# Kernel tuning notes

Measured on AMD Instinct MI355X. Metric: run time of the kernel, lower is better.

## Reference

```python
import jax, jax.numpy as jnp
import numpy as np
import math

D_MODEL = 1024
NUM_HEADS = 16
HEAD_DIM = D_MODEL // NUM_HEADS


def setup_inputs() -> dict:
    key = jax.random.key(0)
    k1, k2, k3, k4 = jax.random.split(key, 4)
    x = jax.random.normal(k1, (1, 4096, D_MODEL), dtype=jnp.float32)
    # torch nn.Linear weights: [out_features, in_features]
    s = 1.0 / math.sqrt(D_MODEL)
    w_qkv = jax.random.uniform(k2, (3 * D_MODEL, D_MODEL), jnp.float32, -s, s)
    w_out = jax.random.uniform(k3, (D_MODEL, D_MODEL), jnp.float32, -s, s)
    b_out = jax.random.uniform(k4, (D_MODEL,), jnp.float32, -s, s)
    return {"x": x, "w_qkv": w_qkv, "w_out": w_out, "b_out": b_out}


def reference(x, w_qkv, w_out, b_out):
    B, T, C = x.shape
    qkv = (x @ w_qkv.T).reshape(B, T, 3, NUM_HEADS, HEAD_DIM)
    q, k, v = qkv[:, :, 0], qkv[:, :, 1], qkv[:, :, 2]  # [B,T,H,Dh]
    scores = jnp.einsum('bthd,bshd->bhts', q, k) / jnp.sqrt(jnp.float32(HEAD_DIM))
    weights = jax.nn.softmax(scores, axis=-1)  # [B,H,T,S]
    attn = jnp.einsum('bhts,bshd->bthd', weights, v).reshape(B, T, C)
    return attn @ w_out.T + b_out
```

## Files before the change

kernel.cpp:

```cpp
#include <hip/hip_runtime.h>
#include <hip/hip_bf16.h>
#include <math.h>

#define T_SEQ 4096
#define NH 16
#define HD 64
#define C_DIM 1024
#define N_QKV 3072

typedef __bf16 bf16x8 __attribute__((ext_vector_type(8)));
typedef __bf16 bf16x2 __attribute__((ext_vector_type(2)));
typedef float f32x4 __attribute__((ext_vector_type(4)));
typedef float f32x16 __attribute__((ext_vector_type(16)));
typedef unsigned short u16x8 __attribute__((ext_vector_type(8)));
typedef unsigned short u16x4 __attribute__((ext_vector_type(4)));
typedef unsigned int u32x4 __attribute__((ext_vector_type(4)));

__device__ __forceinline__ unsigned short f2bf(float f) {
  unsigned u = __builtin_bit_cast(unsigned, f);
  u += 0x7FFFu + ((u >> 16) & 1u);
  return (unsigned short)(u >> 16);
}

__device__ __forceinline__ bf16x8 lds_frag(const unsigned short* p) {
  return __builtin_bit_cast(bf16x8, *reinterpret_cast<const u16x8*>(p));
}

__global__ void convert_kernel(const float* __restrict__ x,
                               const float* __restrict__ wqkv,
                               const float* __restrict__ wout,
                               unsigned short* __restrict__ xb,
                               unsigned short* __restrict__ wqkvb,
                               unsigned short* __restrict__ woutb) {
  const int NX = T_SEQ * C_DIM;
  const int NW = N_QKV * C_DIM;
  const int NO = C_DIM * C_DIM;
  int idx = blockIdx.x * blockDim.x + threadIdx.x;
  int i = idx * 4;
  if (i >= NX + NW + NO) return;
  const float* src;
  unsigned short* dst;
  if (i < NX)            { src = x + i;                dst = xb + i; }
  else if (i < NX + NW)  { src = wqkv + (i - NX);      dst = wqkvb + (i - NX); }
  else                   { src = wout + (i - NX - NW); dst = woutb + (i - NX - NW); }
  float4 v = *reinterpret_cast<const float4*>(src);
  u16x4 o;
  o[0] = f2bf(v.x); o[1] = f2bf(v.y); o[2] = f2bf(v.z); o[3] = f2bf(v.w);
  *reinterpret_cast<u16x4*>(dst) = o;
}

template <bool F32OUT>
__global__ __launch_bounds__(256) void gemm_bt(
    const unsigned short* __restrict__ A, const unsigned short* __restrict__ Bm,
    unsigned short* __restrict__ Cb, float* __restrict__ Cf,
    const float* __restrict__ bias, int M, int N, int K,
    int scale_cols, float ascale) {
  __shared__ __align__(16) unsigned short As[128 * 64];
  __shared__ __align__(16) unsigned short Bs[128 * 64];
  const int tid = threadIdx.x;
  const int lane = tid & 63, wid = tid >> 6;
  const int l15 = lane & 15, g = lane >> 4;
  const int nbn = N >> 7;
  const int bm = blockIdx.x / nbn, bn = blockIdx.x % nbn;
  const int wm = wid >> 1, wn = wid & 1;

  f32x4 acc[4][4];
  const f32x4 zero = {0.f, 0.f, 0.f, 0.f};
#pragma unroll
  for (int m = 0; m < 4; m++)
#pragma unroll
    for (int n = 0; n < 4; n++) acc[m][n] = zero;

  for (int k0 = 0; k0 < K; k0 += 64) {
    __syncthreads();
#pragma unroll
    for (int i = 0; i < 4; i++) {
      int c = tid + i * 256;
      int row = c >> 3, slot = c & 7;
      int b_off = row * 128 + ((slot * 16) ^ ((row & 7) << 4));
      u16x8 va = *reinterpret_cast<const u16x8*>(A + (size_t)(bm * 128 + row) * K + k0 + slot * 8);
      *reinterpret_cast<u16x8*>(reinterpret_cast<char*>(As) + b_off) = va;
      u16x8 vb = *reinterpret_cast<const u16x8*>(Bm + (size_t)(bn * 128 + row) * K + k0 + slot * 8);
      *reinterpret_cast<u16x8*>(reinterpret_cast<char*>(Bs) + b_off) = vb;
    }
    __syncthreads();
#pragma unroll
    for (int kk = 0; kk < 2; kk++) {
      bf16x8 af[4], bfr[4];
#pragma unroll
      for (int m = 0; m < 4; m++) {
        int row = wm * 64 + m * 16 + l15;
        af[m] = lds_frag(reinterpret_cast<const unsigned short*>(
            reinterpret_cast<const char*>(As) + row * 128 + ((kk * 64 + g * 16) ^ ((l15 & 7) << 4))));
      }
#pragma unroll
      for (int n = 0; n < 4; n++) {
        int row = wn * 64 + n * 16 + l15;
        bfr[n] = lds_frag(reinterpret_cast<const unsigned short*>(
            reinterpret_cast<const char*>(Bs) + row * 128 + ((kk * 64 + g * 16) ^ ((l15 & 7) << 4))));
      }
#pragma unroll
      for (int m = 0; m < 4; m++)
#pragma unroll
        for (int n = 0; n < 4; n++)
          acc[m][n] = __builtin_amdgcn_mfma_f32_16x16x32_bf16(af[m], bfr[n], acc[m][n], 0, 0, 0);
    }
  }
#pragma unroll
  for (int m = 0; m < 4; m++) {
    int row0 = bm * 128 + wm * 64 + m * 16 + g * 4;
#pragma unroll
    for (int n = 0; n < 4; n++) {
      int col = bn * 128 + wn * 64 + n * 16 + l15;
      float bi = 0.f;
      if (F32OUT) bi = bias[col];
      float cs = (col < scale_cols) ? ascale : 1.0f;
#pragma unroll
      for (int r = 0; r < 4; r++) {
        float v = acc[m][n][r];
        if (F32OUT) Cf[(size_t)(row0 + r) * N + col] = v + bi;
        else        Cb[(size_t)(row0 + r) * N + col] = f2bf(v * cs);
      }
    }
  }
}

__global__ __launch_bounds__(512, 4) void attn_kernel(
    const unsigned short* __restrict__ qkv,
    unsigned short* __restrict__ attn) {
  __shared__ __align__(16) unsigned short Ksh[2][2][64 * 72];
  __shared__ __align__(16) unsigned short Vsh[2][2][64 * 72];
  const int tid = threadIdx.x;
  const int lane = tid & 63, wid = tid >> 6;
  const int qw = wid & 3, str = wid >> 2;
  const int stid = qw * 64 + lane;
  const int l31 = lane & 31, hi = lane >> 5;
  const int sw = (blockIdx.x & 7) * 64 + (blockIdx.x >> 3);
  const int h = sw >> 5;
  const int qb = sw & 31;
  const int t0 = qb * 128 + qw * 32;
  const int q = l31;
  const int kvbase = str * (T_SEQ / 2);
  const int NT = T_SEQ / 128;

  const int krow = stid >> 3, kslot = stid & 7;
  const int kp = stid & 31, d0 = (stid >> 5) * 8;

  bf16x8 qf[4];
#pragma unroll
  for (int ds = 0; ds < 4; ds++) {
    const unsigned short* p = qkv + (size_t)(t0 + q) * N_QKV + h * HD + ds * 16 + hi * 8;
    qf[ds] = __builtin_bit_cast(bf16x8, *reinterpret_cast<const u16x8*>(p));
  }

  float l_run = 0.f;
  f32x16 o[2];
  const f32x16 zero16 = {0.f};
  o[0] = zero16; o[1] = zero16;
  f32x16 minit;
#pragma unroll
  for (int i = 0; i < 16; i++) minit[i] = -4.0f;

  u16x8 kreg[2], vreg[2];
  {
    const int kv0 = kvbase;
#pragma unroll
    for (int i = 0; i < 2; i++)
      kreg[i] = *reinterpret_cast<const u16x8*>(
          qkv + (size_t)(kv0 + krow + i * 32) * N_QKV + C_DIM + h * HD + kslot * 8);
    const unsigned short* vsrc =
        qkv + (size_t)(kv0 + 2 * kp) * N_QKV + 2 * C_DIM + h * HD + d0;
    vreg[0] = *reinterpret_cast<const u16x8*>(vsrc);
    vreg[1] = *reinterpret_cast<const u16x8*>(vsrc + N_QKV);
  }

  for (int t = 0; t < NT; t++) {
    unsigned short* Kb = Ksh[str][t & 1];
    unsigned short* Vb = Vsh[str][t & 1];
#pragma unroll
    for (int i = 0; i < 2; i++)
      *reinterpret_cast<u16x8*>(&Kb[(krow + i * 32) * 72 + kslot * 8]) = kreg[i];
#pragma unroll
    for (int j = 0; j < 8; j++) {
      unsigned pk = (unsigned)vreg[0][j] | ((unsigned)vreg[1][j] << 16);
      *reinterpret_cast<unsigned*>(&Vb[(d0 + j) * 72 + 2 * kp]) = pk;
    }
    if (t < NT - 1) {
      const int kv0 = kvbase + (t + 1) * 64;
#pragma unroll
      for (int i = 0; i < 2; i++)
        kreg[i] = *reinterpret_cast<const u16x8*>(
            qkv + (size_t)(kv0 + krow + i * 32) * N_QKV + C_DIM + h * HD + kslot * 8);
      const unsigned short* vsrc =
          qkv + (size_t)(kv0 + 2 * kp) * N_QKV + 2 * C_DIM + h * HD + d0;
      vreg[0] = *reinterpret_cast<const u16x8*>(vsrc);
      vreg[1] = *reinterpret_cast<const u16x8*>(vsrc + N_QKV);
    }
    __syncthreads();

    f32x16 s[2];
#pragma unroll
    for (int nt = 0; nt < 2; nt++) {
      s[nt] = minit;
#pragma unroll
      for (int ds = 0; ds < 4; ds++) {
        bf16x8 kf = lds_frag(&Kb[(nt * 32 + l31) * 72 + ds * 16 + hi * 8]);
        s[nt] = __builtin_amdgcn_mfma_f32_32x32x16_bf16(kf, qf[ds], s[nt], 0, 0, 0);
      }
    }

    unsigned wA[2][8];
    float psum[16];
#pragma unroll
    for (int nt = 0; nt < 2; nt++)
#pragma unroll
      for (int i = 0; i < 8; i++) {
        float pa = __builtin_amdgcn_exp2f(s[nt][2 * i]);
        float pb = __builtin_amdgcn_exp2f(s[nt][2 * i + 1]);
        bf16x2 pk = {(__bf16)pa, (__bf16)pb};
        wA[nt][i] = __builtin_bit_cast(unsigned, pk);
        psum[nt * 8 + i] = pa + pb;
      }
#pragma unroll
    for (int i = 0; i < 8; i++) psum[i] += psum[i + 8];
#pragma unroll
    for (int i = 0; i < 4; i++) psum[i] += psum[i + 4];
    l_run += (psum[0] + psum[2]) + (psum[1] + psum[3]);

#pragma unroll
    for (int nt = 0; nt < 2; nt++)
#pragma unroll
      for (int base = 0; base < 8; base += 4)
#pragma unroll
        for (int k = 0; k < 2; k++) {
          unsigned A = wA[nt][base + k];
          unsigned B = wA[nt][base + k + 2];
          unsigned snd = hi ? A : B;
          unsigned rcv = __shfl_xor(snd, 32);
          wA[nt][base + k]     = hi ? rcv : A;
          wA[nt][base + k + 2] = hi ? B   : rcv;
        }

#pragma unroll
    for (int nt = 0; nt < 2; nt++) {
      u32x4 f0 = {wA[nt][0], wA[nt][1], wA[nt][2], wA[nt][3]};
      u32x4 f1 = {wA[nt][4], wA[nt][5], wA[nt][6], wA[nt][7]};
      bf16x8 pf0 = __builtin_bit_cast(bf16x8, f0);
      bf16x8 pf1 = __builtin_bit_cast(bf16x8, f1);
#pragma unroll
      for (int dblk = 0; dblk < 2; dblk++) {
        bf16x8 vf0 = lds_frag(&Vb[(dblk * 32 + l31) * 72 + nt * 32 + hi * 8]);
        o[dblk] = __builtin_amdgcn_mfma_f32_32x32x16_bf16(vf0, pf0, o[dblk], 0, 0, 0);
        bf16x8 vf1 = lds_frag(&Vb[(dblk * 32 + l31) * 72 + nt * 32 + 16 + hi * 8]);
        o[dblk] = __builtin_amdgcn_mfma_f32_32x32x16_bf16(vf1, pf1, o[dblk], 0, 0, 0);
      }
    }
  }

  __syncthreads();
  float* ob = reinterpret_cast<float*>(&Ksh[0][0][0]);
  float* lb = reinterpret_cast<float*>(&Vsh[0][0][0]);
  const int midx = qw * 64 + lane;
  if (str == 1) {
#pragma unroll
    for (int dblk = 0; dblk < 2; dblk++)
#pragma unroll
      for (int r = 0; r < 16; r++)
        ob[(dblk * 16 + r) * 256 + midx] = o[dblk][r];
    lb[midx] = l_run;
  }
  __syncthreads();
  if (str == 0) {
#pragma unroll
    for (int dblk = 0; dblk < 2; dblk++)
#pragma unroll
      for (int r = 0; r < 16; r++)
        o[dblk][r] += ob[(dblk * 16 + r) * 256 + midx];
    l_run += lb[midx];

    float inv = 1.f / (l_run + __shfl_xor(l_run, 32));
    const int t = t0 + q;
#pragma unroll
    for (int dblk = 0; dblk < 2; dblk++)
#pragma unroll
      for (int qd = 0; qd < 4; qd++) {
        u16x4 w;
#pragma unroll
        for (int i = 0; i < 4; i++) w[i] = f2bf(o[dblk][qd * 4 + i] * inv);
        *reinterpret_cast<u16x4*>(
            &attn[(size_t)t * C_DIM + h * HD + dblk * 32 + qd * 8 + hi * 4]) = w;
      }
  }
}

extern "C" void kernel_launch(void* const* d_in, const int* in_sizes, int n_in,
                              void* d_out, int out_size, void* d_ws, size_t ws_size,
                              hipStream_t stream) {
  const float* x     = (const float*)d_in[0];
  const float* w_qkv = (const float*)d_in[1];
  const float* w_out = (const float*)d_in[2];
  const float* b_out = (const float*)d_in[3];
  float* out = (float*)d_out;
  char* ws = (char*)d_ws;
  unsigned short* xb    = (unsigned short*)(ws);
  unsigned short* wqkvb = (unsigned short*)(ws + (8u << 20));
  unsigned short* woutb = (unsigned short*)(ws + (14u << 20));
  unsigned short* qkvb  = (unsigned short*)(ws + (16u << 20));
  unsigned short* attnb = (unsigned short*)(ws + (40u << 20));

  const float QSCALE = 0.125f * 1.44269504f;

  convert_kernel<<<8192, 256, 0, stream>>>(x, w_qkv, w_out, xb, wqkvb, woutb);
  gemm_bt<false><<<768, 256, 0, stream>>>(xb, wqkvb, qkvb, nullptr, nullptr,
                                          T_SEQ, N_QKV, C_DIM, C_DIM, QSCALE);
  attn_kernel<<<512, 512, 0, stream>>>(qkvb, attnb);
  gemm_bt<true><<<256, 256, 0, stream>>>(attnb, woutb, nullptr, out, b_out,
                                         T_SEQ, C_DIM, C_DIM, 0, 1.0f);
}
```

Baseline: 173.9 us.

## Process two query tiles per wave in attention to reuse K/V fragments

```diff
diff --git a/kernel.cpp b/kernel.cpp
--- a/kernel.cpp
+++ b/kernel.cpp
@@ -125,171 +125,201 @@
   }
 }
 
-__global__ __launch_bounds__(512, 4) void attn_kernel(
+__global__ __launch_bounds__(256, 2) void attn_kernel(
     const unsigned short* __restrict__ qkv,
     unsigned short* __restrict__ attn) {
   __shared__ __align__(16) unsigned short Ksh[2][2][64 * 72];
   __shared__ __align__(16) unsigned short Vsh[2][2][64 * 72];
   const int tid = threadIdx.x;
   const int lane = tid & 63, wid = tid >> 6;
-  const int qw = wid & 3, str = wid >> 2;
+  const int qw = wid & 1, str = wid >> 1;
   const int stid = qw * 64 + lane;
   const int l31 = lane & 31, hi = lane >> 5;
   const int sw = (blockIdx.x & 7) * 64 + (blockIdx.x >> 3);
   const int h = sw >> 5;
   const int qb = sw & 31;
-  const int t0 = qb * 128 + qw * 32;
+  const int t0 = qb * 128 + qw * 64;
   const int q = l31;
   const int kvbase = str * (T_SEQ / 2);
   const int NT = T_SEQ / 128;
 
-  const int krow = stid >> 3, kslot = stid & 7;
-  const int kp = stid & 31, d0 = (stid >> 5) * 8;
-
-  bf16x8 qf[4];
-#pragma unroll
-  for (int ds = 0; ds < 4; ds++) {
-    const unsigned short* p = qkv + (size_t)(t0 + q) * N_QKV + h * HD + ds * 16 + hi * 8;
-    qf[ds] = __builtin_bit_cast(bf16x8, *reinterpret_cast<const u16x8*>(p));
-  }
-
-  float l_run = 0.f;
-  f32x16 o[2];
+  const int krow = stid >> 1, ks4 = (stid & 1) * 4;
+  const int kp = stid & 31, d0 = (stid >> 5) * 16;
+
+  bf16x8 qf[2][4];
+#pragma unroll
+  for (int j = 0; j < 2; j++)
+#pragma unroll
+    for (int ds = 0; ds < 4; ds++) {
+      const unsigned short* p =
+          qkv + (size_t)(t0 + j * 32 + q) * N_QKV + h * HD + ds * 16 + hi * 8;
+      qf[j][ds] = __builtin_bit_cast(bf16x8, *reinterpret_cast<const u16x8*>(p));
+    }
+
+  float l_run[2] = {0.f, 0.f};
+  f32x16 o[2][2];
   const f32x16 zero16 = {0.f};
-  o[0] = zero16; o[1] = zero16;
+  o[0][0] = zero16; o[0][1] = zero16; o[1][0] = zero16; o[1][1] = zero16;
   f32x16 minit;
 #pragma unroll
   for (int i = 0; i < 16; i++) minit[i] = -4.0f;
 
-  u16x8 kreg[2], vreg[2];
+  u16x8 kreg[4], vreg[2][2];
   {
     const int kv0 = kvbase;
 #pragma unroll
-    for (int i = 0; i < 2; i++)
+    for (int i = 0; i < 4; i++)
       kreg[i] = *reinterpret_cast<const u16x8*>(
-          qkv + (size_t)(kv0 + krow + i * 32) * N_QKV + C_DIM + h * HD + kslot * 8);
+          qkv + (size_t)(kv0 + krow) * N_QKV + C_DIM + h * HD + (ks4 + i) * 8);
     const unsigned short* vsrc =
         qkv + (size_t)(kv0 + 2 * kp) * N_QKV + 2 * C_DIM + h * HD + d0;
-    vreg[0] = *reinterpret_cast<const u16x8*>(vsrc);
-    vreg[1] = *reinterpret_cast<const u16x8*>(vsrc + N_QKV);
+    vreg[0][0] = *reinterpret_cast<const u16x8*>(vsrc);
+    vreg[0][1] = *reinterpret_cast<const u16x8*>(vsrc + 8);
+    vreg[1][0] = *reinterpret_cast<const u16x8*>(vsrc + N_QKV);
+    vreg[1][1] = *reinterpret_cast<const u16x8*>(vsrc + N_QKV + 8);
   }
 
   for (int t = 0; t < NT; t++) {
     unsigned short* Kb = Ksh[str][t & 1];
     unsigned short* Vb = Vsh[str][t & 1];
 #pragma unroll
-    for (int i = 0; i < 2; i++)
-      *reinterpret_cast<u16x8*>(&Kb[(krow + i * 32) * 72 + kslot * 8]) = kreg[i];
-#pragma unroll
-    for (int j = 0; j < 8; j++) {
-      unsigned pk = (unsigned)vreg[0][j] | ((unsigned)vreg[1][j] << 16);
-      *reinterpret_cast<unsigned*>(&Vb[(d0 + j) * 72 + 2 * kp]) = pk;
-    }
+    for (int i = 0; i < 4; i++)
+      *reinterpret_cast<u16x8*>(&Kb[krow * 72 + (ks4 + i) * 8]) = kreg[i];
+#pragma unroll
+    for (int half = 0; half < 2; half++)
+#pragma unroll
+      for (int jj = 0; jj < 8; jj++) {
+        int d = d0 + half * 8 + jj;
+        unsigned pk = (unsigned)vreg[0][half][jj] | ((unsigned)vreg[1][half][jj] << 16);
+        *reinterpret_cast<unsigned*>(&Vb[d * 72 + 2 * kp]) = pk;
+      }
     if (t < NT - 1) {
       const int kv0 = kvbase + (t + 1) * 64;
 #pragma unroll
-      for (int i = 0; i < 2; i++)
+      for (int i = 0; i < 4; i++)
         kreg[i] = *reinterpret_cast<const u16x8*>(
-            qkv + (size_t)(kv0 + krow + i * 32) * N_QKV + C_DIM + h * HD + kslot * 8);
+            qkv + (size_t)(kv0 + krow) * N_QKV + C_DIM + h * HD + (ks4 + i) * 8);
       const unsigned short* vsrc =
           qkv + (size_t)(kv0 + 2 * kp) * N_QKV + 2 * C_DIM + h * HD + d0;
-      vreg[0] = *reinterpret_cast<const u16x8*>(vsrc);
-      vreg[1] = *reinterpret_cast<const u16x8*>(vsrc + N_QKV);
-    }
-    __syncthreads();
-
-    f32x16 s[2];
-#pragma unroll
-    for (int nt = 0; nt < 2; nt++) {
-      s[nt] = minit;
+      vreg[0][0] = *reinterpret_cast<const u16x8*>(vsrc);
+      vreg[0][1] = *reinterpret_cast<const u16x8*>(vsrc + 8);
+      vreg[1][0] = *reinterpret_cast<const u16x8*>(vsrc + N_QKV);
+      vreg[1][1] = *reinterpret_cast<const u16x8*>(vsrc + N_QKV + 8);
+    }
+    __syncthreads();
+
+    f32x16 s[2][2];
+    s[0][0] = minit; s[0][1] = minit; s[1][0] = minit; s[1][1] = minit;
+#pragma unroll
+    for (int nt = 0; nt < 2; nt++)
 #pragma unroll
       for (int ds = 0; ds < 4; ds++) {
         bf16x8 kf = lds_frag(&Kb[(nt * 32 + l31) * 72 + ds * 16 + hi * 8]);
-        s[nt] = __builtin_amdgcn_mfma_f32_32x32x16_bf16(kf, qf[ds], s[nt], 0, 0, 0);
-      }
-    }
-
-    unsigned wA[2][8];
-    float psum[16];
-#pragma unroll
-    for (int nt = 0; nt < 2; nt++)
-#pragma unroll
-      for (int i = 0; i < 8; i++) {
-        float pa = __builtin_amdgcn_exp2f(s[nt][2 * i]);
-        float pb = __builtin_amdgcn_exp2f(s[nt][2 * i + 1]);
-        bf16x2 pk = {(__bf16)pa, (__bf16)pb};
-        wA[nt][i] = __builtin_bit_cast(unsigned, pk);
-        psum[nt * 8 + i] = pa + pb;
-      }
-#pragma unroll
-    for (int i = 0; i < 8; i++) psum[i] += psum[i + 8];
-#pragma unroll
-    for (int i = 0; i < 4; i++) psum[i] += psum[i + 4];
-    l_run += (psum[0] + psum[2]) + (psum[1] + psum[3]);
-
-#pragma unroll
-    for (int nt = 0; nt < 2; nt++)
-#pragma unroll
-      for (int base = 0; base < 8; base += 4)
-#pragma unroll
-        for (int k = 0; k < 2; k++) {
-          unsigned A = wA[nt][base + k];
-          unsigned B = wA[nt][base + k + 2];
-          unsigned snd = hi ? A : B;
-          unsigned rcv = __shfl_xor(snd, 32);
-          wA[nt][base + k]     = hi ? rcv : A;
-          wA[nt][base + k + 2] = hi ? B   : rcv;
+        s[0][nt] = __builtin_amdgcn_mfma_f32_32x32x16_bf16(kf, qf[0][ds], s[0][nt], 0, 0, 0);
+        s[1][nt] = __builtin_amdgcn_mfma_f32_32x32x16_bf16(kf, qf[1][ds], s[1][nt], 0, 0, 0);
+      }
+
+    unsigned wA[2][2][8];
+#pragma unroll
+    for (int j = 0; j < 2; j++) {
+      float psum[16];
+#pragma unroll
+      for (int nt = 0; nt < 2; nt++)
+#pragma unroll
+        for (int i = 0; i < 8; i++) {
+          float pa = __builtin_amdgcn_exp2f(s[j][nt][2 * i]);
+          float pb = __builtin_amdgcn_exp2f(s[j][nt][2 * i + 1]);
+          bf16x2 pk = {(__bf16)pa, (__bf16)pb};
+          wA[j][nt][i] = __builtin_bit_cast(unsigned, pk);
+          psum[nt * 8 + i] = pa + pb;
         }
+#pragma unroll
+      for (int i = 0; i < 8; i++) psum[i] += psum[i + 8];
+#pragma unroll
+      for (int i = 0; i < 4; i++) psum[i] += psum[i + 4];
+      l_run[j] += (psum[0] + psum[2]) + (psum[1] + psum[3]);
+    }
+
+#pragma unroll
+    for (int j = 0; j < 2; j++)
+#pragma unroll
+      for (int nt = 0; nt < 2; nt++)
+#pragma unroll
+        for (int base = 0; base < 8; base += 4)
+#pragma unroll
+          for (int k = 0; k < 2; k++) {
+            unsigned A = wA[j][nt][base + k];
+            unsigned B = wA[j][nt][base + k + 2];
+            unsigned snd = hi ? A : B;
+            unsigned rcv = __shfl_xor(snd, 32);
+            wA[j][nt][base + k]     = hi ? rcv : A;
+            wA[j][nt][base + k + 2] = hi ? B   : rcv;
+          }
 
 #pragma unroll
     for (int nt = 0; nt < 2; nt++) {
-      u32x4 f0 = {wA[nt][0], wA[nt][1], wA[nt][2], wA[nt][3]};
-      u32x4 f1 = {wA[nt][4], wA[nt][5], wA[nt][6], wA[nt][7]};
-      bf16x8 pf0 = __builtin_bit_cast(bf16x8, f0);
-      bf16x8 pf1 = __builtin_bit_cast(bf16x8, f1);
+      u32x4 g00 = {wA[0][nt][0], wA[0][nt][1], wA[0][nt][2], wA[0][nt][3]};
+      u32x4 g01 = {wA[0][nt][4], wA[0][nt][5], wA[0][nt][6], wA[0][nt][7]};
+      u32x4 g10 = {wA[1][nt][0], wA[1][nt][1], wA[1][nt][2], wA[1][nt][3]};
+      u32x4 g11 = {wA[1][nt][4], wA[1][nt][5], wA[1][nt][6], wA[1][nt][7]};
+      bf16x8 pf00 = __builtin_bit_cast(bf16x8, g00);
+      bf16x8 pf01 = __builtin_bit_cast(bf16x8, g01);
+      bf16x8 pf10 = __builtin_bit_cast(bf16x8, g10);
+      bf16x8 pf11 = __builtin_bit_cast(bf16x8, g11);
 #pragma unroll
       for (int dblk = 0; dblk < 2; dblk++) {
         bf16x8 vf0 = lds_frag(&Vb[(dblk * 32 + l31) * 72 + nt * 32 + hi * 8]);
-        o[dblk] = __builtin_amdgcn_mfma_f32_32x32x16_bf16(vf0, pf0, o[dblk], 0, 0, 0);
         bf16x8 vf1 = lds_frag(&Vb[(dblk * 32 + l31) * 72 + nt * 32 + 16 + hi * 8]);
-        o[dblk] = __builtin_amdgcn_mfma_f32_32x32x16_bf16(vf1, pf1, o[dblk], 0, 0, 0);
-      }
-    }
-  }
-
-  __syncthreads();
+        o[0][dblk] = __builtin_amdgcn_mfma_f32_32x32x16_bf16(vf0, pf00, o[0][dblk], 0, 0, 0);
+        o[0][dblk] = __builtin_amdgcn_mfma_f32_32x32x16_bf16(vf1, pf01, o[0][dblk], 0, 0, 0);
+        o[1][dblk] = __builtin_amdgcn_mfma_f32_32x32x16_bf16(vf0, pf10, o[1][dblk], 0, 0, 0);
+        o[1][dblk] = __builtin_amdgcn_mfma_f32_32x32x16_bf16(vf1, pf11, o[1][dblk], 0, 0, 0);
+      }
+    }
+  }
+
   float* ob = reinterpret_cast<float*>(&Ksh[0][0][0]);
   float* lb = reinterpret_cast<float*>(&Vsh[0][0][0]);
   const int midx = qw * 64 + lane;
-  if (str == 1) {
-#pragma unroll
-    for (int dblk = 0; dblk < 2; dblk++)
-#pragma unroll
-      for (int r = 0; r < 16; r++)
-        ob[(dblk * 16 + r) * 256 + midx] = o[dblk][r];
-    lb[midx] = l_run;
-  }
-  __syncthreads();
+#pragma unroll
+  for (int j = 0; j < 2; j++) {
+    __syncthreads();
+    if (str == 1) {
+#pragma unroll
+      for (int dblk = 0; dblk < 2; dblk++)
+#pragma unroll
+        for (int r = 0; r < 16; r++)
+          ob[(dblk * 16 + r) * 128 + midx] = o[j][dblk][r];
+      lb[midx] = l_run[j];
+    }
+    __syncthreads();
+    if (str == 0) {
+#pragma unroll
+      for (int dblk = 0; dblk < 2; dblk++)
+#pragma unroll
+        for (int r = 0; r < 16; r++)
+          o[j][dblk][r] += ob[(dblk * 16 + r) * 128 + midx];
+      l_run[j] += lb[midx];
+    }
+  }
+
   if (str == 0) {
 #pragma unroll
-    for (int dblk = 0; dblk < 2; dblk++)
-#pragma unroll
-      for (int r = 0; r < 16; r++)
-        o[dblk][r] += ob[(dblk * 16 + r) * 256 + midx];
-    l_run += lb[midx];
-
-    float inv = 1.f / (l_run + __shfl_xor(l_run, 32));
-    const int t = t0 + q;
-#pragma unroll
-    for (int dblk = 0; dblk < 2; dblk++)
-#pragma unroll
-      for (int qd = 0; qd < 4; qd++) {
-        u16x4 w;
-#pragma unroll
-        for (int i = 0; i < 4; i++) w[i] = f2bf(o[dblk][qd * 4 + i] * inv);
-        *reinterpret_cast<u16x4*>(
-            &attn[(size_t)t * C_DIM + h * HD + dblk * 32 + qd * 8 + hi * 4]) = w;
-      }
+    for (int j = 0; j < 2; j++) {
+      float lr = l_run[j];
+      float inv = 1.f / (lr + __shfl_xor(lr, 32));
+      const int t = t0 + j * 32 + q;
+#pragma unroll
+      for (int dblk = 0; dblk < 2; dblk++)
+#pragma unroll
+        for (int qd = 0; qd < 4; qd++) {
+          u16x4 w;
+#pragma unroll
+          for (int i = 0; i < 4; i++) w[i] = f2bf(o[j][dblk][qd * 4 + i] * inv);
+          *reinterpret_cast<u16x4*>(
+              &attn[(size_t)t * C_DIM + h * HD + dblk * 32 + qd * 8 + hi * 4]) = w;
+        }
+    }
   }
 }
 
@@ -313,7 +343,7 @@
   convert_kernel<<<8192, 256, 0, stream>>>(x, w_qkv, w_out, xb, wqkvb, woutb);
   gemm_bt<false><<<768, 256, 0, stream>>>(xb, wqkvb, qkvb, nullptr, nullptr,
                                           T_SEQ, N_QKV, C_DIM, C_DIM, QSCALE);
-  attn_kernel<<<512, 512, 0, stream>>>(qkvb, attnb);
+  attn_kernel<<<512, 256, 0, stream>>>(qkvb, attnb);
   gemm_bt<true><<<256, 256, 0, stream>>>(attnb, woutb, nullptr, out, b_out,
                                          T_SEQ, C_DIM, C_DIM, 0, 1.0f);
 }
```

New measurement: 159.3 us. -8.4%, faster.
